# Performance work log

Hardware: AMD Instinct MI355X
Metric: run time of the kernel (lower is better)

## Reference

```python
import jax, jax.numpy as jnp
import numpy as np


def _rope_tables(T, d):
    half = d // 2
    i = jnp.arange(half, dtype=jnp.float32)
    theta = 10000.0 ** (-2.0 * i / d)          # [half]
    m = jnp.arange(T, dtype=jnp.float32)[:, None]  # [T,1]
    ang = m * theta[None, :]                    # [T,half]
    return jnp.cos(ang), jnp.sin(ang)


def _rotate(v, cos, sin):
    # interleaved even/odd RoPE rotation, vectorized
    B, T, d = v.shape
    half = d // 2
    v2 = v.reshape(B, T, half, 2)
    even, odd = v2[..., 0], v2[..., 1]
    c = cos[None, :, :]
    s = sin[None, :, :]
    new_even = even * c - odd * s
    new_odd = even * s + odd * c
    return jnp.stack([new_even, new_odd], axis=-1).reshape(B, T, d)


def setup_inputs() -> dict:
    key = jax.random.key(0)
    k1, k2, k3, k4 = jax.random.split(key, 4)
    B, T, d = 4, 2048, 1024
    x = jax.random.normal(k1, (B, T, d), dtype=jnp.float32)
    scale = 0.02
    Wq = jax.random.normal(k2, (d, d), dtype=jnp.float32) * scale
    Wk = jax.random.normal(k3, (d, d), dtype=jnp.float32) * scale
    Wv = jax.random.normal(k4, (d, d), dtype=jnp.float32) * scale
    return {"x": x, "Wq": Wq, "Wk": Wk, "Wv": Wv}


def reference(x, Wq, Wk, Wv):
    B, T, d = x.shape
    cos, sin = _rope_tables(T, d)
    # torch Linear: y = x @ W.T
    Q = jnp.einsum('btd,ed->bte', x, Wq)
    K = jnp.einsum('btd,ed->bte', x, Wk)
    V = jnp.einsum('btd,ed->bte', x, Wv)
    Qr = _rotate(Q, cos, sin)
    Kr = _rotate(K, cos, sin)
    scores = jnp.einsum('bqd,bkd->bqk', Qr, Kr) / jnp.sqrt(jnp.float32(d))
    # NOTE: original uses tril with diagonal=1 (allows one future position)
    mask = jnp.tril(jnp.ones((T, T), dtype=bool), k=1)
    scores = jnp.where(mask[None, :, :], scores, -jnp.inf)
    attn = jax.nn.softmax(scores, axis=-1)
    out = jnp.einsum('bqk,bkd->bqd', attn, V)
    return out
```

## Files before the change

### kernel.cpp

```cpp
#include <hip/hip_runtime.h>


typedef float f32x4 __attribute__((ext_vector_type(4)));
typedef __bf16 bf16x8 __attribute__((ext_vector_type(8)));

#define BM 128
#define BN 128
#define BK 64

#define SP_BATCH 2473984

__device__ __forceinline__ unsigned short f2bf(float f) {
  union { float f; unsigned int u; } c; c.f = f;
  unsigned int u = c.u;
  u += 0x7fffu + ((u >> 16) & 1u);
  return (unsigned short)(u >> 16);
}
__device__ __forceinline__ float bf2f(unsigned short h) {
  union { unsigned int u; float f; } c; c.u = ((unsigned int)h) << 16;
  return c.f;
}

__device__ __forceinline__ void async16(const unsigned short* gp, unsigned short* lp) {
  __builtin_amdgcn_global_load_lds(
      (const __attribute__((address_space(1))) void*)gp,
      (__attribute__((address_space(3))) void*)lp, 16, 0, 0);
}

__global__ __launch_bounds__(256) void cvt_all(
    const float4* __restrict__ x, const float4* __restrict__ wq,
    const float4* __restrict__ wk, const float4* __restrict__ wv,
    ushort4* __restrict__ xb, ushort4* __restrict__ wb,
    float4* __restrict__ rowsums) {
  int b = blockIdx.x, t = threadIdx.x;
  if (b == 11264) {
#pragma unroll
    for (int i = 0; i < 8; ++i) rowsums[i * 256 + t] = float4{0.f, 0.f, 0.f, 0.f};
    return;
  }
  const float4* src;
  ushort4* dst;
  long i;
  if (b < 8192) { src = x; dst = xb; i = (long)b * 256 + t; }
  else if (b < 9216) { src = wq; dst = wb; i = (long)(b - 8192) * 256 + t; }
  else if (b < 10240) { src = wk; dst = wb + 262144; i = (long)(b - 9216) * 256 + t; }
  else { src = wv; dst = wb + 524288; i = (long)(b - 10240) * 256 + t; }
  float4 v = src[i];
  ushort4 o;
  o.x = f2bf(v.x); o.y = f2bf(v.y); o.z = f2bf(v.z); o.w = f2bf(v.w);
  dst[i] = o;
}

template <int IM, int JN>
__device__ __forceinline__ void gemm_body(
    const unsigned short* __restrict__ A, const unsigned short* __restrict__ B,
    unsigned short* As, unsigned short* Bs,
    int lda, int ldb, int m0, int n0, int ktiles,
    int tid, int lane, int wave, f32x4 (&acc)[IM][JN]) {
  const int wm = (wave >> 1) * (IM * 16);
  const int wn = (wave & 1) * (JN * 16);
  const int fm = lane & 15;
  const int q = lane >> 4;
  const int srow = tid >> 3;
  const int c = (tid & 7) ^ (srow & 7);
  const unsigned short* Ab = A + (long)(m0 + srow) * lda + c * 8;
  const unsigned short* Bb = B + (long)(n0 + srow) * ldb + c * 8;
  unsigned short* ldA = As + tid * 8;
  unsigned short* ldB = Bs + tid * 8;

  for (int kt = 0; kt < ktiles; ++kt) {
    const long k0 = (long)kt * BK;
    __syncthreads();
#pragma unroll
    for (int p = 0; p < IM; ++p)
      async16(Ab + (long)(p * 32) * lda + k0, ldA + p * 2048);
#pragma unroll
    for (int p = 0; p < JN; ++p)
      async16(Bb + (long)(p * 32) * ldb + k0, ldB + p * 2048);
    __syncthreads();

#pragma unroll
    for (int s = 0; s < 2; ++s) {
      bf16x8 af[IM], bfr[JN];
#pragma unroll
      for (int i = 0; i < IM; ++i) {
        int row = wm + i * 16 + fm;
        af[i] = *(const bf16x8*)&As[row * 64 + ((((s << 2) | q) ^ (row & 7)) << 3)];
      }
#pragma unroll
      for (int j = 0; j < JN; ++j) {
        int row = wn + j * 16 + fm;
        bfr[j] = *(const bf16x8*)&Bs[row * 64 + ((((s << 2) | q) ^ (row & 7)) << 3)];
      }
#pragma unroll
      for (int i = 0; i < IM; ++i)
#pragma unroll
        for (int j = 0; j < JN; ++j)
          acc[i][j] = __builtin_amdgcn_mfma_f32_16x16x32_bf16(af[i], bfr[j], acc[i][j], 0, 0, 0);
    }
  }
}

__global__ __launch_bounds__(256, 3) void qkv_rope_gemm(
    const unsigned short* __restrict__ A, const unsigned short* __restrict__ B,
    unsigned short* __restrict__ Qr, unsigned short* __restrict__ Kr,
    unsigned short* __restrict__ Vt) {
  __shared__ __align__(16) unsigned short As[BM * BK];
  __shared__ __align__(16) unsigned short Bs[BN * BK];
  const int tid = threadIdx.x, lane = tid & 63, wave = tid >> 6;
  const int bm = blockIdx.x, bn = blockIdx.y;
  const int m0 = bm * BM, n0 = bn * BN;
  const int wm = (wave >> 1) * 64, wn = (wave & 1) * 64;
  const int q = lane >> 4, fm = lane & 15;

  f32x4 acc[4][4];
#pragma unroll
  for (int i = 0; i < 4; ++i)
#pragma unroll
    for (int j = 0; j < 4; ++j) acc[i][j] = (f32x4)(0.f);

  gemm_body<4, 4>(A, B, As, Bs, 1024, 1024, m0, n0, 16, tid, lane, wave, acc);

  if (n0 < 2048) {
    const float NEG = -13.287712379549449f / 1024.f;
    unsigned short* dst = (n0 < 1024) ? Qr : Kr;
    const int t00 = (m0 + wm + q * 4) & 2047;
#pragma unroll
    for (int j = 0; j < 4; ++j) {
      int c = (n0 & 1023) + wn + j * 16 + fm;
      float th = exp2f((float)(c & ~1) * NEG);
      float sgn = (c & 1) ? 1.f : -1.f;
      float ang0 = (float)t00 * th;
      float cb = __cosf(ang0), sb = __sinf(ang0);
      float c1 = __cosf(th), s1 = __sinf(th);
      float c16 = __cosf(16.f * th), s16 = __sinf(16.f * th);
#pragma unroll
      for (int i = 0; i < 4; ++i) {
        int gmB = m0 + wm + i * 16 + q * 4;
        float cr = cb, sr = sb;
#pragma unroll
        for (int r = 0; r < 4; ++r) {
          float v = acc[i][j][r];
          float p = __shfl_xor(v, 1);
          dst[(long)(gmB + r) * 1024 + c] = f2bf(v * cr + sgn * p * sr);
          float crn = cr * c1 - sr * s1;
          sr = sr * c1 + cr * s1;
          cr = crn;
        }
        float cbn = cb * c16 - sb * s16;
        sb = sb * c16 + cb * s16;
        cb = cbn;
      }
    }
  } else {
    const int c0 = n0 - 2048;
#pragma unroll
    for (int j = 0; j < 4; ++j) {
      int c = c0 + wn + j * 16 + fm;
#pragma unroll
      for (int i = 0; i < 4; ++i) {
        int gmB = m0 + wm + i * 16 + q * 4;
        int b = gmB >> 11, t = gmB & 2047;
        ushort4 pk;
        pk.x = f2bf(acc[i][j][0]);
        pk.y = f2bf(acc[i][j][1]);
        pk.z = f2bf(acc[i][j][2]);
        pk.w = f2bf(acc[i][j][3]);
        *(ushort4*)&Vt[((long)b * 1024 + c) * 2048 + t] = pk;
      }
    }
  }
}

__global__ __launch_bounds__(256, 3) void s_gemm(
    const unsigned short* __restrict__ Qr, const unsigned short* __restrict__ Kr,
    unsigned short* __restrict__ Sp, float* __restrict__ rowsums) {
  __shared__ __align__(16) unsigned short As[BM * BK];
  __shared__ __align__(16) unsigned short Bs[BN * BK];
  const int tid = threadIdx.x, lane = tid & 63, wave = tid >> 6;
  const int z = blockIdx.z;
  int idx = blockIdx.x, bm = 0;
#pragma unroll 1
  for (; bm < 16; ++bm) {
    int cnt = (bm + 2 > 16) ? 16 : bm + 2;
    if (idx < cnt) break;
    idx -= cnt;
  }
  const int bn = idx;
  const unsigned short* A = Qr + (long)z * 2048 * 1024;
  const unsigned short* B = Kr + (long)z * 2048 * 1024;
  const int len = ((bm + 2 > 16) ? 16 : bm + 2) * 128;
  unsigned short* S = Sp + (long)z * SP_BATCH + (long)(bm * (bm + 3) / 2) * 16384;
  float* rs = rowsums + (long)z * 2048;
  const int m0 = bm * BM, n0 = bn * BN;
  const int wm = (wave >> 1) * 64, wn = (wave & 1) * 64;
  const int q = lane >> 4, fm = lane & 15;

  f32x4 acc[4][4];
#pragma unroll
  for (int i = 0; i < 4; ++i)
#pragma unroll
    for (int j = 0; j < 4; ++j) acc[i][j] = (f32x4)(0.f);

  gemm_body<4, 4>(A, B, As, Bs, 1024, 1024, m0, n0, 16, tid, lane, wave, acc);

  float* rsum = (float*)Bs;
  __syncthreads();
  if (tid < 128) rsum[tid] = 0.f;
  __syncthreads();

#pragma unroll
  for (int i = 0; i < 4; ++i) {
    int gmB = m0 + wm + i * 16 + q * 4;
    int lrow = wm + i * 16 + q * 4;
    float ps[4] = {0.f, 0.f, 0.f, 0.f};
#pragma unroll
    for (int j = 0; j < 4; ++j) {
      int gn = n0 + wn + j * 16 + fm;
#pragma unroll
      for (int r = 0; r < 4; ++r) {
        float e = (gn <= gmB + r + 1) ? __expf(acc[i][j][r] * 0.03125f) : 0.f;
        unsigned short h = f2bf(e);
        S[(long)(lrow + r) * len + gn] = h;
        ps[r] += bf2f(h);
      }
    }
#pragma unroll
    for (int r = 0; r < 4; ++r) {
      float v = ps[r];
      v += __shfl_xor(v, 1);
      v += __shfl_xor(v, 2);
      v += __shfl_xor(v, 4);
      v += __shfl_xor(v, 8);
      if (fm == 0) atomicAdd(&rsum[wm + i * 16 + q * 4 + r], v);
    }
  }
  __syncthreads();
  if (tid < 128) atomicAdd(&rs[m0 + tid], rsum[tid]);
}

__global__ __launch_bounds__(256, 3) void pv_gemm(
    const unsigned short* __restrict__ Sp, const unsigned short* __restrict__ Vt,
    const float* __restrict__ rowsums, float* __restrict__ out) {
  __shared__ __align__(16) unsigned short As[64 * BK];
  __shared__ __align__(16) unsigned short Bs[128 * BK];
  const int tid = threadIdx.x, lane = tid & 63, wave = tid >> 6;
  const int bn = blockIdx.x & 7;
  const int z = blockIdx.x >> 3;
  const int bm = 31 - blockIdx.y;
  const int sb = bm >> 1;
  const int lda = ((sb + 2 > 16) ? 16 : sb + 2) * 128;
  const unsigned short* A = Sp + (long)z * SP_BATCH +
                            (long)(sb * (sb + 3) / 2) * 16384 +
                            (long)(bm & 1) * 64 * lda;
  const unsigned short* B = Vt + (long)z * 1024 * 2048;
  const float* rs = rowsums + (long)z * 2048;
  float* C = out + (long)z * 2048 * 1024;
  int ktiles = bm + 2;
  if (ktiles > 32) ktiles = 32;
  const int m0 = bm * 64, n0 = bn * 128;
  const int wm = (wave >> 1) * 32, wn = (wave & 1) * 64;
  const int q = lane >> 4, fm = lane & 15;

  f32x4 acc[2][4];
#pragma unroll
  for (int i = 0; i < 2; ++i)
#pragma unroll
    for (int j = 0; j < 4; ++j) acc[i][j] = (f32x4)(0.f);

  gemm_body<2, 4>(A, B, As, Bs, lda, 2048, 0, n0, ktiles, tid, lane, wave, acc);

#pragma unroll
  for (int i = 0; i < 2; ++i) {
    int gmB = m0 + wm + i * 16 + q * 4;
#pragma unroll
    for (int r = 0; r < 4; ++r) {
      float inv = 1.f / rs[gmB + r];
#pragma unroll
      for (int j = 0; j < 4; ++j) {
        int gn = n0 + wn + j * 16 + fm;
        C[(long)(gmB + r) * 1024 + gn] = acc[i][j][r] * inv;
      }
    }
  }
}

extern "C" void kernel_launch(void* const* d_in, const int* in_sizes, int n_in,
                              void* d_out, int out_size, void* d_ws, size_t ws_size,
                              hipStream_t stream) {
  const float* x = (const float*)d_in[0];
  const float* Wq = (const float*)d_in[1];
  const float* Wk = (const float*)d_in[2];
  const float* Wv = (const float*)d_in[3];
  float* out = (float*)d_out;

  float* rowsums = (float*)d_ws;
  unsigned short* Qr = (unsigned short*)d_ws + 16384;
  unsigned short* Kr = Qr + (long)8192 * 1024;
  unsigned short* Vt = Kr + (long)8192 * 1024;
  unsigned short* xb = Vt + (long)8192 * 1024;
  unsigned short* Wb = xb + (long)8192 * 1024;

  cvt_all<<<11265, 256, 0, stream>>>((const float4*)x, (const float4*)Wq,
                                     (const float4*)Wk, (const float4*)Wv,
                                     (ushort4*)xb, (ushort4*)Wb, (float4*)rowsums);

  qkv_rope_gemm<<<dim3(64, 24), 256, 0, stream>>>(xb, Wb, Qr, Kr, Vt);

  unsigned short* Sp = xb;
  s_gemm<<<dim3(151, 1, 4), 256, 0, stream>>>(Qr, Kr, Sp, rowsums);
  pv_gemm<<<dim3(32, 32), 256, 0, stream>>>(Sp, Vt, rowsums, out);
}
```

Before: 222.3 us.

## Split score GEMM into 64-row tiles, zero-fill fully masked tiles, raise occupancy hints

```diff
diff --git a/kernel.cpp b/kernel.cpp
--- a/kernel.cpp
+++ b/kernel.cpp
@@ -101,7 +101,7 @@
   }
 }
 
-__global__ __launch_bounds__(256, 3) void qkv_rope_gemm(
+__global__ __launch_bounds__(256, 4) void qkv_rope_gemm(
     const unsigned short* __restrict__ A, const unsigned short* __restrict__ B,
     unsigned short* __restrict__ Qr, unsigned short* __restrict__ Kr,
     unsigned short* __restrict__ Vt) {
@@ -172,47 +172,61 @@
   }
 }
 
-__global__ __launch_bounds__(256, 3) void s_gemm(
+__global__ __launch_bounds__(256, 4) void s_gemm(
     const unsigned short* __restrict__ Qr, const unsigned short* __restrict__ Kr,
     unsigned short* __restrict__ Sp, float* __restrict__ rowsums) {
-  __shared__ __align__(16) unsigned short As[BM * BK];
+  __shared__ __align__(16) unsigned short As[64 * BK];
   __shared__ __align__(16) unsigned short Bs[BN * BK];
   const int tid = threadIdx.x, lane = tid & 63, wave = tid >> 6;
   const int z = blockIdx.z;
-  int idx = blockIdx.x, bm = 0;
+  int idx = blockIdx.x, b = 31;
 #pragma unroll 1
-  for (; bm < 16; ++bm) {
-    int cnt = (bm + 2 > 16) ? 16 : bm + 2;
+  for (; b > 0; --b) {
+    int cnt = ((b >> 1) + 2 > 16) ? 16 : (b >> 1) + 2;
     if (idx < cnt) break;
     idx -= cnt;
   }
   const int bn = idx;
+  const int sb = b >> 1;
+  const int len = ((sb + 2 > 16) ? 16 : sb + 2) * 128;
+  unsigned short* S = Sp + (long)z * SP_BATCH + (long)(sb * (sb + 3) / 2) * 16384 +
+                      (long)(b & 1) * 64 * len;
+
+  if (128 * bn > 64 * b + 64) {
+    ushort4 zz{0, 0, 0, 0};
+#pragma unroll
+    for (int u = 0; u < 8; ++u) {
+      int e = tid * 8 + u;
+      int row = e >> 5, c4 = e & 31;
+      *(ushort4*)&S[(long)row * len + bn * 128 + c4 * 4] = zz;
+    }
+    return;
+  }
+
   const unsigned short* A = Qr + (long)z * 2048 * 1024;
   const unsigned short* B = Kr + (long)z * 2048 * 1024;
-  const int len = ((bm + 2 > 16) ? 16 : bm + 2) * 128;
-  unsigned short* S = Sp + (long)z * SP_BATCH + (long)(bm * (bm + 3) / 2) * 16384;
   float* rs = rowsums + (long)z * 2048;
-  const int m0 = bm * BM, n0 = bn * BN;
-  const int wm = (wave >> 1) * 64, wn = (wave & 1) * 64;
+  const int m0 = b * 64, n0 = bn * 128;
+  const int wm = (wave >> 1) * 32, wn = (wave & 1) * 64;
   const int q = lane >> 4, fm = lane & 15;
 
-  f32x4 acc[4][4];
-#pragma unroll
-  for (int i = 0; i < 4; ++i)
+  f32x4 acc[2][4];
+#pragma unroll
+  for (int i = 0; i < 2; ++i)
 #pragma unroll
     for (int j = 0; j < 4; ++j) acc[i][j] = (f32x4)(0.f);
 
-  gemm_body<4, 4>(A, B, As, Bs, 1024, 1024, m0, n0, 16, tid, lane, wave, acc);
+  gemm_body<2, 4>(A, B, As, Bs, 1024, 1024, m0, n0, 16, tid, lane, wave, acc);
 
   float* rsum = (float*)Bs;
   __syncthreads();
-  if (tid < 128) rsum[tid] = 0.f;
+  if (tid < 64) rsum[tid] = 0.f;
   __syncthreads();
 
 #pragma unroll
-  for (int i = 0; i < 4; ++i) {
-    int gmB = m0 + wm + i * 16 + q * 4;
-    int lrow = wm + i * 16 + q * 4;
+  for (int i = 0; i < 2; ++i) {
+    int lr = wm + i * 16 + q * 4;
+    int gmB = m0 + lr;
     float ps[4] = {0.f, 0.f, 0.f, 0.f};
 #pragma unroll
     for (int j = 0; j < 4; ++j) {
@@ -221,7 +235,7 @@
       for (int r = 0; r < 4; ++r) {
         float e = (gn <= gmB + r + 1) ? __expf(acc[i][j][r] * 0.03125f) : 0.f;
         unsigned short h = f2bf(e);
-        S[(long)(lrow + r) * len + gn] = h;
+        S[(long)(lr + r) * len + gn] = h;
         ps[r] += bf2f(h);
       }
     }
@@ -232,14 +246,14 @@
       v += __shfl_xor(v, 2);
       v += __shfl_xor(v, 4);
       v += __shfl_xor(v, 8);
-      if (fm == 0) atomicAdd(&rsum[wm + i * 16 + q * 4 + r], v);
+      if (fm == 0) atomicAdd(&rsum[lr + r], v);
     }
   }
   __syncthreads();
-  if (tid < 128) atomicAdd(&rs[m0 + tid], rsum[tid]);
-}
-
-__global__ __launch_bounds__(256, 3) void pv_gemm(
+  if (tid < 64) atomicAdd(&rs[m0 + tid], rsum[tid]);
+}
+
+__global__ __launch_bounds__(256, 4) void pv_gemm(
     const unsigned short* __restrict__ Sp, const unsigned short* __restrict__ Vt,
     const float* __restrict__ rowsums, float* __restrict__ out) {
   __shared__ __align__(16) unsigned short As[64 * BK];
@@ -308,6 +322,6 @@
   qkv_rope_gemm<<<dim3(64, 24), 256, 0, stream>>>(xb, Wb, Qr, Kr, Vt);
 
   unsigned short* Sp = xb;
-  s_gemm<<<dim3(151, 1, 4), 256, 0, stream>>>(Qr, Kr, Sp, rowsums);
+  s_gemm<<<dim3(302, 1, 4), 256, 0, stream>>>(Qr, Kr, Sp, rowsums);
   pv_gemm<<<dim3(32, 32), 256, 0, stream>>>(Sp, Vt, rowsums, out);
 }
```

Result: no change. 219.2 us (-1.4%).
